# Optimization experiments

Measured on AMD Instinct MI355X. Metric: run time of the kernel, lower is better.

## Reference

```python
import jax, jax.numpy as jnp
import numpy as np

N, IN_DIM, H_DIM, POS_DIM, K, M, E, OUT_DIM = 50000, 256, 96, 32, 64, 128, 800000, 40
HID = H_DIM + POS_DIM  # 128

def _lin(key, fan_out, fan_in):
    k1, k2 = jax.random.split(key)
    bnd = 1.0 / np.sqrt(fan_in)
    W = jax.random.uniform(k1, (fan_out, fan_in), minval=-bnd, maxval=bnd, dtype=jnp.float32)
    b = jax.random.uniform(k2, (fan_out,), minval=-bnd, maxval=bnd, dtype=jnp.float32)
    return W, b

def setup_inputs() -> dict:
    key = jax.random.key(0)
    ks = jax.random.split(key, 12)
    x = jax.random.normal(ks[0], (N, IN_DIM), dtype=jnp.float32)
    eigenvectors = jax.random.normal(ks[1], (N, M), dtype=jnp.float32)
    eigenvalues = jax.random.uniform(ks[2], (M,), dtype=jnp.float32)
    edge_index = jax.random.randint(ks[3], (2, E), 0, N, dtype=jnp.int64)
    W_feat, b_feat = _lin(ks[4], H_DIM, IN_DIM)
    alpha = jax.random.uniform(ks[5], (K, POS_DIM), minval=-1/np.sqrt(K), maxval=1/np.sqrt(K), dtype=jnp.float32)
    Wl1, bl1 = _lin(ks[6], HID, HID)
    Wr1, _ = _lin(ks[7], HID, HID)
    Wl2, bl2 = _lin(ks[8], HID, HID)
    Wr2, _ = _lin(ks[9], HID, HID)
    W_ro, b_ro = _lin(ks[10], OUT_DIM, HID)
    return dict(x=x, eigenvectors=eigenvectors, eigenvalues=eigenvalues, edge_index=edge_index,
                W_feat=W_feat, b_feat=b_feat, alpha=alpha,
                Wl1=Wl1, bl1=bl1, Wr1=Wr1, Wl2=Wl2, bl2=bl2, Wr2=Wr2,
                W_ro=W_ro, b_ro=b_ro)

def _sage_conv(x, src, dst, Wl, bl, Wr):
    # PyG SAGEConv (mean aggr): out = lin_l(mean_{j->i} x_j) + lin_r(x_i)
    n = x.shape[0]
    agg = jax.ops.segment_sum(x[src], dst, num_segments=n)           # [N, HID]
    cnt = jax.ops.segment_sum(jnp.ones_like(dst, dtype=x.dtype), dst, num_segments=n)
    mean = agg / jnp.maximum(cnt, 1.0)[:, None]
    return mean @ Wl.T + bl + x @ Wr.T

def reference(x, eigenvectors, eigenvalues, edge_index,
              W_feat, b_feat, alpha, Wl1, bl1, Wr1, Wl2, bl2, Wr2, W_ro, b_ro):
    # normalize eigenvectors per column to [-1, 1]
    ev_min = jnp.min(eigenvectors, axis=0, keepdims=True)
    ev_max = jnp.max(eigenvectors, axis=0, keepdims=True)
    ev = (eigenvectors - ev_min) / (ev_max - ev_min) * 2.0 - 1.0
    # normalize eigenvalues to [-1, 1], Chebyshev basis via arccos/cos
    lmin, lmax = jnp.min(eigenvalues), jnp.max(eigenvalues)
    lam = (eigenvalues - lmin) / (lmax - lmin) * 2.0 - 1.0
    theta = jnp.arccos(lam)[:, None] * jnp.arange(K, dtype=lam.dtype)[None, :]  # [M, K]
    pe = jnp.cos(theta) @ alpha                                                  # [M, pos_dim]
    pos = ev @ pe                                                                # [N, pos_dim]
    h = jnp.concatenate([x @ W_feat.T + b_feat, pos], axis=-1)                   # [N, HID]
    src, dst = edge_index[0], edge_index[1]
    h = jax.nn.relu(_sage_conv(h, src, dst, Wl1, bl1, Wr1))
    h = jax.nn.relu(_sage_conv(h, src, dst, Wl2, bl2, Wr2))
    out = jax.nn.log_softmax(h @ W_ro.T + b_ro, axis=-1)
    return out, pe
```

## Files before the change

kernel.cpp:

```cpp
#include <hip/hip_runtime.h>
#include <math.h>

#define N        50000
#define IN_DIM   256
#define H_DIM    96
#define POS_DIM  32
#define KCH      64
#define M        128
#define NE       800000
#define OUT_DIM  40
#define HID      128
#define NSCAN    196
#define NTILES   ((N + 63) / 64)
#define NBK      391
#define BKCAP    2560
#define NSCATB   512
#define SREG     1563

typedef __attribute__((ext_vector_type(8))) short short8v;
typedef __attribute__((ext_vector_type(4))) float float4v;

__device__ __forceinline__ unsigned short f2bf(float f){
  unsigned u = __float_as_uint(f);
  u += 0x7fffu + ((u >> 16) & 1u);
  return (unsigned short)(u >> 16);
}
__device__ __forceinline__ float bf_lo(unsigned u){ return __uint_as_float(u << 16); }
__device__ __forceinline__ float bf_hi(unsigned u){ return __uint_as_float(u & 0xffff0000u); }

__device__ __forceinline__ unsigned enc_key(float f){
  unsigned u = __float_as_uint(f);
  return (u & 0x80000000u) ? ~u : (u | 0x80000000u);
}
__device__ __forceinline__ float dec_key(unsigned k){
  unsigned u = (k & 0x80000000u) ? (k ^ 0x80000000u) : ~k;
  return __uint_as_float(u);
}

__global__ void k_init(unsigned* __restrict__ encmn, unsigned* __restrict__ encmx,
                       short* __restrict__ WT_pos, float* __restrict__ bias_pos,
                       int* __restrict__ bkt_cnt){
  int i = blockIdx.x*blockDim.x + threadIdx.x;
  if (i < M){ encmn[i] = 0xFFFFFFFFu; encmx[i] = 0u; bias_pos[i] = 0.f; }
  if (i < M*M) WT_pos[i] = 0;
  if (i < NBK) bkt_cnt[i] = 0;
}

__global__ __launch_bounds__(256) void k_colminmax(const float* __restrict__ ev,
    unsigned* __restrict__ encmn, unsigned* __restrict__ encmx){
  __shared__ float4 smn[256], smx[256];
  int tid = threadIdx.x;
  int cg  = tid & 31;
  int rs  = blockIdx.x*8 + (tid >> 5);
  int stride = gridDim.x*8;
  float4 mn = make_float4( 3.4e38f,  3.4e38f,  3.4e38f,  3.4e38f);
  float4 mx = make_float4(-3.4e38f, -3.4e38f, -3.4e38f, -3.4e38f);
  #pragma unroll 4
  for (int r = rs; r < N; r += stride){
    float4 v = *(const float4*)&ev[(size_t)r*M + cg*4];
    mn.x = fminf(mn.x, v.x); mn.y = fminf(mn.y, v.y);
    mn.z = fminf(mn.z, v.z); mn.w = fminf(mn.w, v.w);
    mx.x = fmaxf(mx.x, v.x); mx.y = fmaxf(mx.y, v.y);
    mx.z = fmaxf(mx.z, v.z); mx.w = fmaxf(mx.w, v.w);
  }
  smn[tid] = mn; smx[tid] = mx;
  __syncthreads();
  for (int s = 128; s >= 32; s >>= 1){
    if (tid < s){
      float4 a = smn[tid], b = smn[tid + s];
      smn[tid] = make_float4(fminf(a.x,b.x), fminf(a.y,b.y), fminf(a.z,b.z), fminf(a.w,b.w));
      float4 c = smx[tid], d = smx[tid + s];
      smx[tid] = make_float4(fmaxf(c.x,d.x), fmaxf(c.y,d.y), fmaxf(c.z,d.z), fmaxf(c.w,d.w));
    }
    __syncthreads();
  }
  if (tid < 32){
    float4 a = smn[tid], b = smx[tid];
    atomicMin(&encmn[tid*4+0], enc_key(a.x));
    atomicMin(&encmn[tid*4+1], enc_key(a.y));
    atomicMin(&encmn[tid*4+2], enc_key(a.z));
    atomicMin(&encmn[tid*4+3], enc_key(a.w));
    atomicMax(&encmx[tid*4+0], enc_key(b.x));
    atomicMax(&encmx[tid*4+1], enc_key(b.y));
    atomicMax(&encmx[tid*4+2], enc_key(b.z));
    atomicMax(&encmx[tid*4+3], enc_key(b.w));
  }
}

__global__ __launch_bounds__(256) void k_pe(
    const float* __restrict__ eigval, const float* __restrict__ alpha,
    const unsigned* __restrict__ encmn, const unsigned* __restrict__ encmx,
    short* __restrict__ WT_pos, float* __restrict__ pe_raw,
    float* __restrict__ pe_out){
  __shared__ float rmn[128], rmx[128];
  int tid = threadIdx.x;
  if (tid < 128){ float v = eigval[tid]; rmn[tid] = v; rmx[tid] = v; }
  __syncthreads();
  for (int s = 64; s; s >>= 1){
    if (tid < s){ rmn[tid] = fminf(rmn[tid], rmn[tid+s]); rmx[tid] = fmaxf(rmx[tid], rmx[tid+s]); }
    __syncthreads();
  }
  float lmin = rmn[0], lmax = rmx[0];
  int g = blockIdx.x*256 + tid;
  int m = g >> 5, p = g & 31;
  float v = eigval[m];
  float lam = (v - lmin)/(lmax - lmin)*2.0f - 1.0f;
  lam = fminf(1.0f, fmaxf(-1.0f, lam));
  float t0 = 1.0f, t1 = lam;
  float acc = alpha[p] + lam*alpha[POS_DIM + p];
  float two_lam = lam + lam;
  #pragma unroll
  for (int k = 2; k < KCH; ++k){
    float t2 = fmaf(two_lam, t1, -t0);
    acc = fmaf(t2, alpha[k*POS_DIM + p], acc);
    t0 = t1; t1 = t2;
  }
  pe_out[g] = acc;
  pe_raw[g] = acc;
  float cmn = dec_key(encmn[m]);
  float cmx = dec_key(encmx[m]);
  float A = 2.0f/(cmx - cmn);
  WT_pos[p*M + m] = (short)f2bf(A*acc);
}

__global__ __launch_bounds__(256) void k_bias(
    const unsigned* __restrict__ encmn, const unsigned* __restrict__ encmx,
    const float* __restrict__ pe_raw, float* __restrict__ bias_pos){
  __shared__ float s[256];
  int tid = threadIdx.x;
  int p = tid >> 3, c = tid & 7;
  float sum = 0.f;
  for (int m = c*16; m < c*16 + 16; ++m){
    float cmn = dec_key(encmn[m]);
    float cmx = dec_key(encmx[m]);
    float A = 2.0f/(cmx - cmn);
    float B = -cmn*A - 1.0f;
    sum += B*pe_raw[m*POS_DIM + p];
  }
  s[tid] = sum;
  __syncthreads();
  if (c == 0){
    float t = 0.f;
    #pragma unroll
    for (int j = 0; j < 8; ++j) t += s[p*8 + j];
    bias_pos[p] = t;
  }
}

__global__ void k_prep_w(const float* __restrict__ Wf, const float* __restrict__ bfeat,
                         const float* __restrict__ Wl1, const float* __restrict__ Wr1,
                         const float* __restrict__ Wl2, const float* __restrict__ Wr2,
                         const float* __restrict__ Wro, const float* __restrict__ bro,
                         short* __restrict__ WTf, float* __restrict__ biasf,
                         short* __restrict__ Wc1, short* __restrict__ Wc2,
                         short* __restrict__ WTro, float* __restrict__ biasro){
  int i = blockIdx.x*256 + threadIdx.x;
  if (i < 128*256){
    int c = i >> 8, k = i & 255;
    WTf[i] = (c < H_DIM) ? (short)f2bf(Wf[c*IN_DIM + k]) : (short)0;
    Wc1[i] = (short)f2bf((k < HID) ? Wl1[c*HID + k] : Wr1[c*HID + k - HID]);
    Wc2[i] = (short)f2bf((k < HID) ? Wl2[c*HID + k] : Wr2[c*HID + k - HID]);
  }
  if (i < 48*128){
    int c = i >> 7, k = i & 127;
    WTro[i] = (c < OUT_DIM) ? (short)f2bf(Wro[c*HID + k]) : (short)0;
  }
  if (i < 128) biasf[i] = (i < H_DIM) ? bfeat[i] : 0.f;
  if (i >= 128 && i < 176) biasro[i - 128] = (i - 128 < OUT_DIM) ? bro[i - 128] : 0.f;
}

__global__ __launch_bounds__(256) void k_gemm_in(
    const float* __restrict__ x, const float* __restrict__ ev,
    const short* __restrict__ WTf, const float* __restrict__ biasf,
    const short* __restrict__ WT_pos, const float* __restrict__ bias_pos,
    unsigned short* __restrict__ outp)
{
  __shared__ short a_lds[64*384];
  int tid = threadIdx.x;
  int wid = tid >> 6, lane = tid & 63;
  int lrow = lane & 15, lk = (lane >> 4)*8;
  bool isPos = (wid == 3);

  short8v bfragF[8][2];
  short8v bfragP[4][2];
  float b0, b1;
  if (!isPos){
    int colBase = wid*32;
    #pragma unroll
    for (int s = 0; s < 8; ++s)
      #pragma unroll
      for (int ct = 0; ct < 2; ++ct){
        int col = colBase + ct*16 + lrow;
        bfragF[s][ct] = *(const short8v*)&WTf[col*256 + s*32 + lk];
      }
    b0 = biasf[colBase + lrow]; b1 = biasf[colBase + 16 + lrow];
  } else {
    #pragma unroll
    for (int s = 0; s < 4; ++s)
      #pragma unroll
      for (int ct = 0; ct < 2; ++ct){
        int col = ct*16 + lrow;
        bfragP[s][ct] = *(const short8v*)&WT_pos[col*128 + s*32 + lk];
      }
    b0 = bias_pos[lrow]; b1 = bias_pos[16 + lrow];
  }

  for (int tile = blockIdx.x; tile < NTILES; tile += gridDim.x){
    int n0 = tile*64;
    __syncthreads();
    for (int c = tid; c < 64*48; c += 256){
      int row = c / 48, k8 = c % 48;
      int gn = min(n0 + row, N-1);
      const float* src = (k8 < 32) ? &x[(size_t)gn*IN_DIM + k8*8]
                                   : &ev[(size_t)gn*M + (k8-32)*8];
      float4v f0 = *(const float4v*)src;
      float4v f1 = *(const float4v*)(src + 4);
      short8v vv;
      vv[0] = (short)f2bf(f0[0]); vv[1] = (short)f2bf(f0[1]);
      vv[2] = (short)f2bf(f0[2]); vv[3] = (short)f2bf(f0[3]);
      vv[4] = (short)f2bf(f1[0]); vv[5] = (short)f2bf(f1[1]);
      vv[6] = (short)f2bf(f1[2]); vv[7] = (short)f2bf(f1[3]);
      unsigned off = (unsigned)(row*768 + k8*16) ^ (unsigned)((row & 7) << 4);
      *(short8v*)((char*)a_lds + off) = vv;
    }
    __syncthreads();
    float4v acc[4][2];
    #pragma unroll
    for (int nt = 0; nt < 4; ++nt){
      acc[nt][0] = (float4v){0.f,0.f,0.f,0.f};
      acc[nt][1] = (float4v){0.f,0.f,0.f,0.f};
    }
    if (!isPos){
      #pragma unroll
      for (int s = 0; s < 8; ++s)
        #pragma unroll
        for (int nt = 0; nt < 4; ++nt){
          int row = nt*16 + lrow;
          unsigned off = (unsigned)(row*768 + (s*32 + lk)*2) ^ (unsigned)((row & 7) << 4);
          short8v a = *(const short8v*)((const char*)a_lds + off);
          acc[nt][0] = __builtin_amdgcn_mfma_f32_16x16x32_bf16(a, bfragF[s][0], acc[nt][0], 0, 0, 0);
          acc[nt][1] = __builtin_amdgcn_mfma_f32_16x16x32_bf16(a, bfragF[s][1], acc[nt][1], 0, 0, 0);
        }
    } else {
      #pragma unroll
      for (int s = 0; s < 4; ++s)
        #pragma unroll
        for (int nt = 0; nt < 4; ++nt){
          int row = nt*16 + lrow;
          unsigned off = (unsigned)(row*768 + 512 + (s*32 + lk)*2) ^ (unsigned)((row & 7) << 4);
          short8v a = *(const short8v*)((const char*)a_lds + off);
          acc[nt][0] = __builtin_amdgcn_mfma_f32_16x16x32_bf16(a, bfragP[s][0], acc[nt][0], 0, 0, 0);
          acc[nt][1] = __builtin_amdgcn_mfma_f32_16x16x32_bf16(a, bfragP[s][1], acc[nt][1], 0, 0, 0);
        }
    }
    int colBase = isPos ? 96 : wid*32;
    int rbase = (lane >> 4)*4;
    #pragma unroll
    for (int nt = 0; nt < 4; ++nt)
      #pragma unroll
      for (int ct = 0; ct < 2; ++ct){
        int col = colBase + ct*16 + lrow;
        float bb = ct ? b1 : b0;
        #pragma unroll
        for (int r = 0; r < 4; ++r){
          int node = n0 + nt*16 + rbase + r;
          if (node < N) outp[(size_t)node*HID + col] = f2bf(acc[nt][ct][r] + bb);
        }
      }
  }
}

__global__ __launch_bounds__(256) void k_conv(
    const short* __restrict__ A0, const short* __restrict__ A1,
    const short* __restrict__ WT, const float* __restrict__ bias,
    unsigned short* __restrict__ outp)
{
  __shared__ short a_lds[64*256];
  int tid = threadIdx.x;
  int wid = tid >> 6, lane = tid & 63;
  int colBase = wid*32;
  int lrow = lane & 15, lk = (lane >> 4)*8;

  short8v bfrag[8][2];
  #pragma unroll
  for (int s = 0; s < 8; ++s)
    #pragma unroll
    for (int ct = 0; ct < 2; ++ct){
      int col = colBase + ct*16 + lrow;
      bfrag[s][ct] = *(const short8v*)&WT[col*256 + s*32 + lk];
    }
  float b0 = bias[colBase + lrow], b1 = bias[colBase + 16 + lrow];

  for (int tile = blockIdx.x; tile < NTILES; tile += gridDim.x){
    int n0 = tile*64;
    __syncthreads();
    #pragma unroll
    for (int c = tid; c < 64*32; c += 256){
      int row = c >> 5, k8 = c & 31;
      int gn = min(n0 + row, N-1);
      const short* src = (k8 < 16) ? (A0 + (size_t)gn*HID + k8*8)
                                   : (A1 + (size_t)gn*HID + (k8-16)*8);
      short8v vv = *(const short8v*)src;
      unsigned off = (unsigned)(row*512 + k8*16) ^ (unsigned)((row & 7) << 4);
      *(short8v*)((char*)a_lds + off) = vv;
    }
    __syncthreads();
    float4v acc[4][2];
    #pragma unroll
    for (int nt = 0; nt < 4; ++nt){
      acc[nt][0] = (float4v){0.f,0.f,0.f,0.f};
      acc[nt][1] = (float4v){0.f,0.f,0.f,0.f};
    }
    #pragma unroll
    for (int s = 0; s < 8; ++s)
      #pragma unroll
      for (int nt = 0; nt < 4; ++nt){
        int row = nt*16 + lrow;
        unsigned off = (unsigned)(row*512 + (s*32 + lk)*2) ^ (unsigned)((row & 7) << 4);
        short8v a = *(const short8v*)((const char*)a_lds + off);
        acc[nt][0] = __builtin_amdgcn_mfma_f32_16x16x32_bf16(a, bfrag[s][0], acc[nt][0], 0, 0, 0);
        acc[nt][1] = __builtin_amdgcn_mfma_f32_16x16x32_bf16(a, bfrag[s][1], acc[nt][1], 0, 0, 0);
      }
    int rbase = (lane >> 4)*4;
    #pragma unroll
    for (int nt = 0; nt < 4; ++nt)
      #pragma unroll
      for (int ct = 0; ct < 2; ++ct){
        int col = colBase + ct*16 + lrow;
        float bb = ct ? b1 : b0;
        #pragma unroll
        for (int r = 0; r < 4; ++r){
          int node = n0 + nt*16 + rbase + r;
          if (node < N)
            outp[(size_t)node*HID + col] = f2bf(fmaxf(acc[nt][ct][r] + bb, 0.f));
        }
      }
  }
}

__global__ __launch_bounds__(256) void k_conv_ro(
    const short* __restrict__ A0, const short* __restrict__ A1,
    const short* __restrict__ WT, const float* __restrict__ bias,
    const short* __restrict__ WTro, const float* __restrict__ biasro,
    float* __restrict__ out)
{
  __shared__ short a_lds[64*256];
  __shared__ short o_lds[64*128];
  int tid = threadIdx.x;
  int wid = tid >> 6, lane = tid & 63;
  int colBase = wid*32;
  int lrow = lane & 15, lk = (lane >> 4)*8;

  short8v bfrag[8][2];
  #pragma unroll
  for (int s = 0; s < 8; ++s)
    #pragma unroll
    for (int ct = 0; ct < 2; ++ct){
      int col = colBase + ct*16 + lrow;
      bfrag[s][ct] = *(const short8v*)&WT[col*256 + s*32 + lk];
    }
  float b0 = bias[colBase + lrow], b1 = bias[colBase + 16 + lrow];

  short8v bfragR[4][3];
  #pragma unroll
  for (int s = 0; s < 4; ++s)
    #pragma unroll
    for (int t = 0; t < 3; ++t){
      int col = t*16 + lrow;
      bfragR[s][t] = *(const short8v*)&WTro[col*HID + s*32 + lk];
    }
  float biasR[3] = { biasro[lrow], biasro[16 + lrow], biasro[32 + lrow] };
  bool val2 = lrow < 8;

  for (int tile = blockIdx.x; tile < NTILES; tile += gridDim.x){
    int n0 = tile*64;
    __syncthreads();
    #pragma unroll
    for (int c = tid; c < 64*32; c += 256){
      int row = c >> 5, k8 = c & 31;
      int gn = min(n0 + row, N-1);
      const short* src = (k8 < 16) ? (A0 + (size_t)gn*HID + k8*8)
                                   : (A1 + (size_t)gn*HID + (k8-16)*8);
      short8v vv = *(const short8v*)src;
      unsigned off = (unsigned)(row*512 + k8*16) ^ (unsigned)((row & 7) << 4);
      *(short8v*)((char*)a_lds + off) = vv;
    }
    __syncthreads();
    float4v acc[4][2];
    #pragma unroll
    for (int nt = 0; nt < 4; ++nt){
      acc[nt][0] = (float4v){0.f,0.f,0.f,0.f};
      acc[nt][1] = (float4v){0.f,0.f,0.f,0.f};
    }
    #pragma unroll
    for (int s = 0; s < 8; ++s)
      #pragma unroll
      for (int nt = 0; nt < 4; ++nt){
        int row = nt*16 + lrow;
        unsigned off = (unsigned)(row*512 + (s*32 + lk)*2) ^ (unsigned)((row & 7) << 4);
        short8v a = *(const short8v*)((const char*)a_lds + off);
        acc[nt][0] = __builtin_amdgcn_mfma_f32_16x16x32_bf16(a, bfrag[s][0], acc[nt][0], 0, 0, 0);
        acc[nt][1] = __builtin_amdgcn_mfma_f32_16x16x32_bf16(a, bfrag[s][1], acc[nt][1], 0, 0, 0);
      }
    int rbase = (lane >> 4)*4;
    #pragma unroll
    for (int nt = 0; nt < 4; ++nt)
      #pragma unroll
      for (int ct = 0; ct < 2; ++ct){
        int col = colBase + ct*16 + lrow;
        float bb = ct ? b1 : b0;
        #pragma unroll
        for (int r = 0; r < 4; ++r){
          int row = nt*16 + rbase + r;
          float v = fmaxf(acc[nt][ct][r] + bb, 0.f);
          unsigned off = (unsigned)(row*256 + col*2) ^ (unsigned)((row & 7) << 4);
          *(short*)((char*)o_lds + off) = (short)f2bf(v);
        }
      }
    __syncthreads();
    float4v acc3[3];
    acc3[0] = (float4v){0.f,0.f,0.f,0.f};
    acc3[1] = (float4v){0.f,0.f,0.f,0.f};
    acc3[2] = (float4v){0.f,0.f,0.f,0.f};
    #pragma unroll
    for (int s = 0; s < 4; ++s){
      int row = wid*16 + lrow;
      unsigned off = (unsigned)(row*256 + (s*32 + lk)*2) ^ (unsigned)((row & 7) << 4);
      short8v a = *(const short8v*)((const char*)o_lds + off);
      acc3[0] = __builtin_amdgcn_mfma_f32_16x16x32_bf16(a, bfragR[s][0], acc3[0], 0, 0, 0);
      acc3[1] = __builtin_amdgcn_mfma_f32_16x16x32_bf16(a, bfragR[s][1], acc3[1], 0, 0, 0);
      acc3[2] = __builtin_amdgcn_mfma_f32_16x16x32_bf16(a, bfragR[s][2], acc3[2], 0, 0, 0);
    }
    #pragma unroll
    for (int r = 0; r < 4; ++r){
      float v0 = acc3[0][r] + biasR[0];
      float v1 = acc3[1][r] + biasR[1];
      float v2 = acc3[2][r] + biasR[2];
      float mx = fmaxf(v0, v1);
      mx = fmaxf(mx, val2 ? v2 : -3.4e38f);
      #pragma unroll
      for (int off = 1; off < 16; off <<= 1) mx = fmaxf(mx, __shfl_xor(mx, off, 64));
      float e = expf(v0 - mx) + expf(v1 - mx) + (val2 ? expf(v2 - mx) : 0.f);
      #pragma unroll
      for (int off = 1; off < 16; off <<= 1) e += __shfl_xor(e, off, 64);
      float lz = mx + logf(e);
      int node = n0 + wid*16 + (lane >> 4)*4 + r;
      if (node < N){
        out[(size_t)node*OUT_DIM + lrow]      = v0 - lz;
        out[(size_t)node*OUT_DIM + 16 + lrow] = v1 - lz;
        if (val2) out[(size_t)node*OUT_DIM + 32 + lrow] = v2 - lz;
      }
    }
  }
}

__global__ __launch_bounds__(256) void k_hist(const int* __restrict__ dst,
                                              int* __restrict__ bkt_cnt){
  __shared__ int h[NBK];
  int tid = threadIdx.x;
  for (int i = tid; i < NBK; i += 256) h[i] = 0;
  __syncthreads();
  for (int e = blockIdx.x*256 + tid; e < NE; e += gridDim.x*256)
    atomicAdd(&h[dst[e] >> 7], 1);
  __syncthreads();
  for (int i = tid; i < NBK; i += 256){
    int c = h[i];
    if (c) atomicAdd(&bkt_cnt[i], c);
  }
}

__global__ __launch_bounds__(512) void k_bktscan(const int* __restrict__ bkt_cnt,
    int* __restrict__ bkt_start, int* __restrict__ bkt_cursor){
  __shared__ int s[512];
  int t = threadIdx.x;
  int v = (t < NBK) ? bkt_cnt[t] : 0;
  s[t] = v;
  __syncthreads();
  for (int st = 1; st < 512; st <<= 1){
    int a = (t >= st) ? s[t-st] : 0;
    __syncthreads();
    s[t] += a;
    __syncthreads();
  }
  int excl = s[t] - v;
  if (t < NBK){ bkt_start[t] = excl; bkt_cursor[t] = excl; }
  if (t == 0) bkt_start[NBK] = NE;
}

__global__ __launch_bounds__(256) void k_bscatter(const int* __restrict__ src,
    const int* __restrict__ dst, int* __restrict__ bkt_cursor,
    unsigned* __restrict__ estage){
  __shared__ int lcnt[NBK];
  __shared__ int lbase[NBK];
  int tid = threadIdx.x;
  int e0 = blockIdx.x*SREG;
  int e1 = min(e0 + SREG, NE);
  for (int i = tid; i < NBK; i += 256) lcnt[i] = 0;
  __syncthreads();
  for (int e = e0 + tid; e < e1; e += 256)
    atomicAdd(&lcnt[dst[e] >> 7], 1);
  __syncthreads();
  for (int i = tid; i < NBK; i += 256){
    int c = lcnt[i];
    lbase[i] = c ? atomicAdd(&bkt_cursor[i], c) : 0;
    lcnt[i] = 0;
  }
  __syncthreads();
  for (int e = e0 + tid; e < e1; e += 256){
    int d = dst[e];
    int b = d >> 7;
    int slot = lbase[b] + atomicAdd(&lcnt[b], 1);
    estage[slot] = (unsigned)src[e] | ((unsigned)(d & 127) << 16);
  }
}

__global__ __launch_bounds__(256) void k_bcsr(const int* __restrict__ bkt_start,
    const unsigned* __restrict__ estage, unsigned short* __restrict__ csr,
    int* __restrict__ row_ptr){
  __shared__ unsigned eb[BKCAP];
  __shared__ int ncnt[128], sc[128], noff[128];
  int tid = threadIdx.x;
  int b = blockIdx.x;
  int s = bkt_start[b], e = bkt_start[b+1];
  int cnt = min(e - s, BKCAP);
  for (int i = tid; i < cnt; i += 256) eb[i] = estage[s + i];
  if (tid < 128) ncnt[tid] = 0;
  __syncthreads();
  for (int i = tid; i < cnt; i += 256)
    atomicAdd(&ncnt[(eb[i] >> 16) & 127], 1);
  __syncthreads();
  if (tid < 128) sc[tid] = ncnt[tid];
  __syncthreads();
  for (int st = 1; st < 128; st <<= 1){
    int a = (tid < 128 && tid >= st) ? sc[tid-st] : 0;
    __syncthreads();
    if (tid < 128) sc[tid] += a;
    __syncthreads();
  }
  if (tid < 128){
    int excl = sc[tid] - ncnt[tid];
    noff[tid] = excl;
    int node = b*128 + tid;
    if (node <= N) row_ptr[node] = s + excl;
    ncnt[tid] = 0;
  }
  __syncthreads();
  for (int i = tid; i < cnt; i += 256){
    unsigned v = eb[i];
    int ld = (v >> 16) & 127;
    int slot = noff[ld] + atomicAdd(&ncnt[ld], 1);
    csr[s + slot] = (unsigned short)(v & 0xffffu);
  }
}

__global__ __launch_bounds__(256) void k_agg_b(const unsigned* __restrict__ h,
    const int* __restrict__ row_ptr, const unsigned short* __restrict__ csr,
    unsigned* __restrict__ outm){
  int gid = blockIdx.x*blockDim.x + threadIdx.x;
  int i = gid >> 6;
  int lane = gid & 63;
  if (i >= N) return;
  int grp = lane >> 4;
  int lc  = lane & 15;
  int b = row_ptr[i], e = row_ptr[i+1];
  float a0[8] = {0.f,0.f,0.f,0.f,0.f,0.f,0.f,0.f};
  float a1[8] = {0.f,0.f,0.f,0.f,0.f,0.f,0.f,0.f};
  int j = b + grp;
  for (; j + 4 < e; j += 8){
    int s0 = csr[j];
    int s1 = csr[j+4];
    uint4 v0 = *(const uint4*)&h[(size_t)s0*64 + lc*4];
    uint4 v1 = *(const uint4*)&h[(size_t)s1*64 + lc*4];
    a0[0] += bf_lo(v0.x); a0[1] += bf_hi(v0.x);
    a0[2] += bf_lo(v0.y); a0[3] += bf_hi(v0.y);
    a0[4] += bf_lo(v0.z); a0[5] += bf_hi(v0.z);
    a0[6] += bf_lo(v0.w); a0[7] += bf_hi(v0.w);
    a1[0] += bf_lo(v1.x); a1[1] += bf_hi(v1.x);
    a1[2] += bf_lo(v1.y); a1[3] += bf_hi(v1.y);
    a1[4] += bf_lo(v1.z); a1[5] += bf_hi(v1.z);
    a1[6] += bf_lo(v1.w); a1[7] += bf_hi(v1.w);
  }
  if (j < e){
    int s0 = csr[j];
    uint4 v0 = *(const uint4*)&h[(size_t)s0*64 + lc*4];
    a0[0] += bf_lo(v0.x); a0[1] += bf_hi(v0.x);
    a0[2] += bf_lo(v0.y); a0[3] += bf_hi(v0.y);
    a0[4] += bf_lo(v0.z); a0[5] += bf_hi(v0.z);
    a0[6] += bf_lo(v0.w); a0[7] += bf_hi(v0.w);
  }
  #pragma unroll
  for (int k = 0; k < 8; ++k){
    float t = a0[k] + a1[k];
    t += __shfl_xor(t, 16, 64);
    t += __shfl_xor(t, 32, 64);
    a0[k] = t;
  }
  if (grp == 0){
    float inv = 1.0f / fmaxf((float)(e - b), 1.0f);
    uint4 o;
    o.x = (unsigned)f2bf(a0[0]*inv) | ((unsigned)f2bf(a0[1]*inv) << 16);
    o.y = (unsigned)f2bf(a0[2]*inv) | ((unsigned)f2bf(a0[3]*inv) << 16);
    o.z = (unsigned)f2bf(a0[4]*inv) | ((unsigned)f2bf(a0[5]*inv) << 16);
    o.w = (unsigned)f2bf(a0[6]*inv) | ((unsigned)f2bf(a0[7]*inv) << 16);
    *(uint4*)&outm[(size_t)i*64 + lc*4] = o;
  }
}

extern "C" void kernel_launch(void* const* d_in, const int* in_sizes, int n_in,
                              void* d_out, int out_size, void* d_ws, size_t ws_size,
                              hipStream_t stream){
  const float* x     = (const float*)d_in[0];
  const float* ev    = (const float*)d_in[1];
  const float* eigv  = (const float*)d_in[2];
  const int*   ei    = (const int*)d_in[3];
  const float* Wf    = (const float*)d_in[4];
  const float* bf    = (const float*)d_in[5];
  const float* alpha = (const float*)d_in[6];
  const float* Wl1   = (const float*)d_in[7];
  const float* bl1   = (const float*)d_in[8];
  const float* Wr1   = (const float*)d_in[9];
  const float* Wl2   = (const float*)d_in[10];
  const float* bl2   = (const float*)d_in[11];
  const float* Wr2   = (const float*)d_in[12];
  const float* Wro   = (const float*)d_in[13];
  const float* bro   = (const float*)d_in[14];
  float* out = (float*)d_out;

  short* h0b    = (short*)d_ws;
  short* h1b    = h0b + (size_t)N*HID;
  short* meanb  = h1b + (size_t)N*HID;
  short* WTf    = meanb + (size_t)N*HID;
  short* Wc1    = WTf + 128*256;
  short* Wc2    = Wc1 + 128*256;
  short* WT_pos = Wc2 + 128*256;
  short* WTro   = WT_pos + 128*128;
  float* biasf    = (float*)(WTro + 48*128);
  float* bias_pos = biasf + 128;
  float* biasro   = bias_pos + 128;
  unsigned* encmn = (unsigned*)(biasro + 48);
  unsigned* encmx = encmn + M;
  int* bkt_cnt    = (int*)(encmx + M);
  int* bkt_start  = bkt_cnt + NBK;
  int* bkt_cursor = bkt_start + NBK + 1;
  int* row_ptr    = bkt_cursor + NBK;
  unsigned* estage = (unsigned*)(row_ptr + N + 1);
  unsigned short* csr = (unsigned short*)(estage + NE);
  float* pe_raw = (float*)(csr + NE);

  const int* srcA = ei;
  const int* dstA = ei + NE;

  k_init<<<NSCAN, 256, 0, stream>>>(encmn, encmx, WT_pos, bias_pos, bkt_cnt);
  k_colminmax<<<256, 256, 0, stream>>>(ev, encmn, encmx);
  k_pe<<<16, 256, 0, stream>>>(eigv, alpha, encmn, encmx, WT_pos, pe_raw,
                               out + (size_t)N*OUT_DIM);
  k_bias<<<1, 256, 0, stream>>>(encmn, encmx, pe_raw, bias_pos);
  k_prep_w<<<128, 256, 0, stream>>>(Wf, bf, Wl1, Wr1, Wl2, Wr2, Wro, bro,
                                    WTf, biasf, Wc1, Wc2, WTro, biasro);
  k_hist<<<512, 256, 0, stream>>>(dstA, bkt_cnt);
  k_bktscan<<<1, 512, 0, stream>>>(bkt_cnt, bkt_start, bkt_cursor);
  k_bscatter<<<NSCATB, 256, 0, stream>>>(srcA, dstA, bkt_cursor, estage);
  k_bcsr<<<NBK, 256, 0, stream>>>(bkt_start, estage, csr, row_ptr);
  k_gemm_in<<<NTILES, 256, 0, stream>>>(x, ev, WTf, biasf, WT_pos, bias_pos,
                                        (unsigned short*)h0b);
  k_agg_b<<<(N*64)/256, 256, 0, stream>>>((const unsigned*)h0b, row_ptr, csr, (unsigned*)meanb);
  k_conv<<<NTILES, 256, 0, stream>>>(meanb, h0b, Wc1, bl1, (unsigned short*)h1b);
  k_agg_b<<<(N*64)/256, 256, 0, stream>>>((const unsigned*)h1b, row_ptr, csr, (unsigned*)meanb);
  k_conv_ro<<<NTILES, 256, 0, stream>>>(meanb, h1b, Wc2, bl2, WTro, biasro, out);
}
```

Baseline: 225.4 us.

## Merge independent preprocessing kernels into block-partitioned fused launches; unroll aggregation deeper

Independent preprocessing stages are combined into shared launches, with blocks split by blockIdx: column min/max with the edge histogram, PE/weight prep with the bucket scan, scatter with the bias reduction, and CSR build with the input GEMM. This cuts the launch count from 11 to 5 before aggregation, which reduces launch gaps and lets small kernels run alongside larger ones. The aggregation kernel now keeps four independent neighbour loads in flight instead of two to raise memory-level parallelism. In exchange, the fused blocks are heterogeneous and bring larger LDS and register footprints, and the GEMM now runs with a grid-stride offset.

```diff
diff --git a/kernel.cpp b/kernel.cpp
--- a/kernel.cpp
+++ b/kernel.cpp
@@ -38,145 +38,240 @@
 }
 
 __global__ void k_init(unsigned* __restrict__ encmn, unsigned* __restrict__ encmx,
-                       short* __restrict__ WT_pos, float* __restrict__ bias_pos,
-                       int* __restrict__ bkt_cnt){
+                       short* __restrict__ WT_pos, int* __restrict__ bkt_cnt){
   int i = blockIdx.x*blockDim.x + threadIdx.x;
-  if (i < M){ encmn[i] = 0xFFFFFFFFu; encmx[i] = 0u; bias_pos[i] = 0.f; }
+  if (i < M){ encmn[i] = 0xFFFFFFFFu; encmx[i] = 0u; }
   if (i < M*M) WT_pos[i] = 0;
   if (i < NBK) bkt_cnt[i] = 0;
 }
 
-__global__ __launch_bounds__(256) void k_colminmax(const float* __restrict__ ev,
-    unsigned* __restrict__ encmn, unsigned* __restrict__ encmx){
-  __shared__ float4 smn[256], smx[256];
+__global__ __launch_bounds__(256) void k_f1(const float* __restrict__ ev,
+    unsigned* __restrict__ encmn, unsigned* __restrict__ encmx,
+    const int* __restrict__ dst, int* __restrict__ bkt_cnt){
   int tid = threadIdx.x;
-  int cg  = tid & 31;
-  int rs  = blockIdx.x*8 + (tid >> 5);
-  int stride = gridDim.x*8;
-  float4 mn = make_float4( 3.4e38f,  3.4e38f,  3.4e38f,  3.4e38f);
-  float4 mx = make_float4(-3.4e38f, -3.4e38f, -3.4e38f, -3.4e38f);
-  #pragma unroll 4
-  for (int r = rs; r < N; r += stride){
-    float4 v = *(const float4*)&ev[(size_t)r*M + cg*4];
-    mn.x = fminf(mn.x, v.x); mn.y = fminf(mn.y, v.y);
-    mn.z = fminf(mn.z, v.z); mn.w = fminf(mn.w, v.w);
-    mx.x = fmaxf(mx.x, v.x); mx.y = fmaxf(mx.y, v.y);
-    mx.z = fmaxf(mx.z, v.z); mx.w = fmaxf(mx.w, v.w);
-  }
-  smn[tid] = mn; smx[tid] = mx;
-  __syncthreads();
-  for (int s = 128; s >= 32; s >>= 1){
-    if (tid < s){
-      float4 a = smn[tid], b = smn[tid + s];
-      smn[tid] = make_float4(fminf(a.x,b.x), fminf(a.y,b.y), fminf(a.z,b.z), fminf(a.w,b.w));
-      float4 c = smx[tid], d = smx[tid + s];
-      smx[tid] = make_float4(fmaxf(c.x,d.x), fmaxf(c.y,d.y), fmaxf(c.z,d.z), fmaxf(c.w,d.w));
-    }
-    __syncthreads();
-  }
-  if (tid < 32){
-    float4 a = smn[tid], b = smx[tid];
-    atomicMin(&encmn[tid*4+0], enc_key(a.x));
-    atomicMin(&encmn[tid*4+1], enc_key(a.y));
-    atomicMin(&encmn[tid*4+2], enc_key(a.z));
-    atomicMin(&encmn[tid*4+3], enc_key(a.w));
-    atomicMax(&encmx[tid*4+0], enc_key(b.x));
-    atomicMax(&encmx[tid*4+1], enc_key(b.y));
-    atomicMax(&encmx[tid*4+2], enc_key(b.z));
-    atomicMax(&encmx[tid*4+3], enc_key(b.w));
-  }
-}
-
-__global__ __launch_bounds__(256) void k_pe(
+  if (blockIdx.x < 256){
+    __shared__ float4 smn[256], smx[256];
+    int cg  = tid & 31;
+    int rs  = blockIdx.x*8 + (tid >> 5);
+    float4 mn = make_float4( 3.4e38f,  3.4e38f,  3.4e38f,  3.4e38f);
+    float4 mx = make_float4(-3.4e38f, -3.4e38f, -3.4e38f, -3.4e38f);
+    #pragma unroll 4
+    for (int r = rs; r < N; r += 2048){
+      float4 v = *(const float4*)&ev[(size_t)r*M + cg*4];
+      mn.x = fminf(mn.x, v.x); mn.y = fminf(mn.y, v.y);
+      mn.z = fminf(mn.z, v.z); mn.w = fminf(mn.w, v.w);
+      mx.x = fmaxf(mx.x, v.x); mx.y = fmaxf(mx.y, v.y);
+      mx.z = fmaxf(mx.z, v.z); mx.w = fmaxf(mx.w, v.w);
+    }
+    smn[tid] = mn; smx[tid] = mx;
+    __syncthreads();
+    for (int s = 128; s >= 32; s >>= 1){
+      if (tid < s){
+        float4 a = smn[tid], b = smn[tid + s];
+        smn[tid] = make_float4(fminf(a.x,b.x), fminf(a.y,b.y), fminf(a.z,b.z), fminf(a.w,b.w));
+        float4 c = smx[tid], d = smx[tid + s];
+        smx[tid] = make_float4(fmaxf(c.x,d.x), fmaxf(c.y,d.y), fmaxf(c.z,d.z), fmaxf(c.w,d.w));
+      }
+      __syncthreads();
+    }
+    if (tid < 32){
+      float4 a = smn[tid], b = smx[tid];
+      atomicMin(&encmn[tid*4+0], enc_key(a.x));
+      atomicMin(&encmn[tid*4+1], enc_key(a.y));
+      atomicMin(&encmn[tid*4+2], enc_key(a.z));
+      atomicMin(&encmn[tid*4+3], enc_key(a.w));
+      atomicMax(&encmx[tid*4+0], enc_key(b.x));
+      atomicMax(&encmx[tid*4+1], enc_key(b.y));
+      atomicMax(&encmx[tid*4+2], enc_key(b.z));
+      atomicMax(&encmx[tid*4+3], enc_key(b.w));
+    }
+  } else {
+    __shared__ int hh[NBK];
+    int bid = blockIdx.x - 256;
+    for (int i = tid; i < NBK; i += 256) hh[i] = 0;
+    __syncthreads();
+    for (int e = bid*256 + tid; e < NE; e += 512*256)
+      atomicAdd(&hh[dst[e] >> 7], 1);
+    __syncthreads();
+    for (int i = tid; i < NBK; i += 256){
+      int c = hh[i];
+      if (c) atomicAdd(&bkt_cnt[i], c);
+    }
+  }
+}
+
+__global__ __launch_bounds__(512) void k_f2(
     const float* __restrict__ eigval, const float* __restrict__ alpha,
     const unsigned* __restrict__ encmn, const unsigned* __restrict__ encmx,
-    short* __restrict__ WT_pos, float* __restrict__ pe_raw,
-    float* __restrict__ pe_out){
-  __shared__ float rmn[128], rmx[128];
+    const float* __restrict__ Wf, const float* __restrict__ bfeat,
+    const float* __restrict__ Wl1, const float* __restrict__ Wr1,
+    const float* __restrict__ Wl2, const float* __restrict__ Wr2,
+    const float* __restrict__ Wro, const float* __restrict__ bro,
+    short* __restrict__ WT_pos, float* __restrict__ pe_raw, float* __restrict__ pe_out,
+    short* __restrict__ WTf, float* __restrict__ biasf,
+    short* __restrict__ Wc1, short* __restrict__ Wc2,
+    short* __restrict__ WTro, float* __restrict__ biasro,
+    const int* __restrict__ bkt_cnt, int* __restrict__ bkt_start,
+    int* __restrict__ bkt_cursor){
   int tid = threadIdx.x;
-  if (tid < 128){ float v = eigval[tid]; rmn[tid] = v; rmx[tid] = v; }
-  __syncthreads();
-  for (int s = 64; s; s >>= 1){
-    if (tid < s){ rmn[tid] = fminf(rmn[tid], rmn[tid+s]); rmx[tid] = fmaxf(rmx[tid], rmx[tid+s]); }
-    __syncthreads();
-  }
-  float lmin = rmn[0], lmax = rmx[0];
-  int g = blockIdx.x*256 + tid;
-  int m = g >> 5, p = g & 31;
-  float v = eigval[m];
-  float lam = (v - lmin)/(lmax - lmin)*2.0f - 1.0f;
-  lam = fminf(1.0f, fmaxf(-1.0f, lam));
-  float t0 = 1.0f, t1 = lam;
-  float acc = alpha[p] + lam*alpha[POS_DIM + p];
-  float two_lam = lam + lam;
-  #pragma unroll
-  for (int k = 2; k < KCH; ++k){
-    float t2 = fmaf(two_lam, t1, -t0);
-    acc = fmaf(t2, alpha[k*POS_DIM + p], acc);
-    t0 = t1; t1 = t2;
-  }
-  pe_out[g] = acc;
-  pe_raw[g] = acc;
-  float cmn = dec_key(encmn[m]);
-  float cmx = dec_key(encmx[m]);
-  float A = 2.0f/(cmx - cmn);
-  WT_pos[p*M + m] = (short)f2bf(A*acc);
-}
-
-__global__ __launch_bounds__(256) void k_bias(
-    const unsigned* __restrict__ encmn, const unsigned* __restrict__ encmx,
-    const float* __restrict__ pe_raw, float* __restrict__ bias_pos){
-  __shared__ float s[256];
-  int tid = threadIdx.x;
-  int p = tid >> 3, c = tid & 7;
-  float sum = 0.f;
-  for (int m = c*16; m < c*16 + 16; ++m){
+  if (blockIdx.x < 8){
+    __shared__ float rmn[128], rmx[128];
+    if (tid < 128){ float v = eigval[tid]; rmn[tid] = v; rmx[tid] = v; }
+    __syncthreads();
+    for (int s = 64; s; s >>= 1){
+      if (tid < s){ rmn[tid] = fminf(rmn[tid], rmn[tid+s]); rmx[tid] = fmaxf(rmx[tid], rmx[tid+s]); }
+      __syncthreads();
+    }
+    float lmin = rmn[0], lmax = rmx[0];
+    int g = blockIdx.x*512 + tid;
+    int m = g >> 5, p = g & 31;
+    float v = eigval[m];
+    float lam = (v - lmin)/(lmax - lmin)*2.0f - 1.0f;
+    lam = fminf(1.0f, fmaxf(-1.0f, lam));
+    float t0 = 1.0f, t1 = lam;
+    float acc = alpha[p] + lam*alpha[POS_DIM + p];
+    float two_lam = lam + lam;
+    #pragma unroll
+    for (int k = 2; k < KCH; ++k){
+      float t2 = fmaf(two_lam, t1, -t0);
+      acc = fmaf(t2, alpha[k*POS_DIM + p], acc);
+      t0 = t1; t1 = t2;
+    }
+    pe_out[g] = acc;
+    pe_raw[g] = acc;
     float cmn = dec_key(encmn[m]);
     float cmx = dec_key(encmx[m]);
     float A = 2.0f/(cmx - cmn);
-    float B = -cmn*A - 1.0f;
-    sum += B*pe_raw[m*POS_DIM + p];
-  }
-  s[tid] = sum;
-  __syncthreads();
-  if (c == 0){
-    float t = 0.f;
-    #pragma unroll
-    for (int j = 0; j < 8; ++j) t += s[p*8 + j];
-    bias_pos[p] = t;
-  }
-}
-
-__global__ void k_prep_w(const float* __restrict__ Wf, const float* __restrict__ bfeat,
-                         const float* __restrict__ Wl1, const float* __restrict__ Wr1,
-                         const float* __restrict__ Wl2, const float* __restrict__ Wr2,
-                         const float* __restrict__ Wro, const float* __restrict__ bro,
-                         short* __restrict__ WTf, float* __restrict__ biasf,
-                         short* __restrict__ Wc1, short* __restrict__ Wc2,
-                         short* __restrict__ WTro, float* __restrict__ biasro){
-  int i = blockIdx.x*256 + threadIdx.x;
-  if (i < 128*256){
-    int c = i >> 8, k = i & 255;
-    WTf[i] = (c < H_DIM) ? (short)f2bf(Wf[c*IN_DIM + k]) : (short)0;
-    Wc1[i] = (short)f2bf((k < HID) ? Wl1[c*HID + k] : Wr1[c*HID + k - HID]);
-    Wc2[i] = (short)f2bf((k < HID) ? Wl2[c*HID + k] : Wr2[c*HID + k - HID]);
-  }
-  if (i < 48*128){
-    int c = i >> 7, k = i & 127;
-    WTro[i] = (c < OUT_DIM) ? (short)f2bf(Wro[c*HID + k]) : (short)0;
-  }
-  if (i < 128) biasf[i] = (i < H_DIM) ? bfeat[i] : 0.f;
-  if (i >= 128 && i < 176) biasro[i - 128] = (i - 128 < OUT_DIM) ? bro[i - 128] : 0.f;
-}
-
-__global__ __launch_bounds__(256) void k_gemm_in(
+    WT_pos[p*M + m] = (short)f2bf(A*acc);
+    for (int i = g; i < 128*256; i += 4096){
+      int c = i >> 8, k = i & 255;
+      WTf[i] = (c < H_DIM) ? (short)f2bf(Wf[c*IN_DIM + k]) : (short)0;
+      Wc1[i] = (short)f2bf((k < HID) ? Wl1[c*HID + k] : Wr1[c*HID + k - HID]);
+      Wc2[i] = (short)f2bf((k < HID) ? Wl2[c*HID + k] : Wr2[c*HID + k - HID]);
+    }
+    for (int i = g; i < 48*128; i += 4096){
+      int c = i >> 7, k = i & 127;
+      WTro[i] = (c < OUT_DIM) ? (short)f2bf(Wro[c*HID + k]) : (short)0;
+    }
+    if (g < 128) biasf[g] = (g < H_DIM) ? bfeat[g] : 0.f;
+    if (g >= 128 && g < 176) biasro[g - 128] = (g - 128 < OUT_DIM) ? bro[g - 128] : 0.f;
+  } else {
+    __shared__ int s[512];
+    int t = tid;
+    int v = (t < NBK) ? bkt_cnt[t] : 0;
+    s[t] = v;
+    __syncthreads();
+    for (int st = 1; st < 512; st <<= 1){
+      int a = (t >= st) ? s[t-st] : 0;
+      __syncthreads();
+      s[t] += a;
+      __syncthreads();
+    }
+    int excl = s[t] - v;
+    if (t < NBK){ bkt_start[t] = excl; bkt_cursor[t] = excl; }
+    if (t == 0) bkt_start[NBK] = NE;
+  }
+}
+
+__global__ __launch_bounds__(256) void k_f3(const int* __restrict__ src,
+    const int* __restrict__ dst, int* __restrict__ bkt_cursor,
+    unsigned* __restrict__ estage,
+    const unsigned* __restrict__ encmn, const unsigned* __restrict__ encmx,
+    const float* __restrict__ pe_raw, float* __restrict__ bias_pos){
+  int tid = threadIdx.x;
+  if (blockIdx.x < NSCATB){
+    __shared__ int lcnt[NBK];
+    __shared__ int lbase[NBK];
+    int e0 = blockIdx.x*SREG;
+    int e1 = min(e0 + SREG, NE);
+    for (int i = tid; i < NBK; i += 256) lcnt[i] = 0;
+    __syncthreads();
+    for (int e = e0 + tid; e < e1; e += 256)
+      atomicAdd(&lcnt[dst[e] >> 7], 1);
+    __syncthreads();
+    for (int i = tid; i < NBK; i += 256){
+      int c = lcnt[i];
+      lbase[i] = c ? atomicAdd(&bkt_cursor[i], c) : 0;
+      lcnt[i] = 0;
+    }
+    __syncthreads();
+    for (int e = e0 + tid; e < e1; e += 256){
+      int d = dst[e];
+      int b = d >> 7;
+      int slot = lbase[b] + atomicAdd(&lcnt[b], 1);
+      estage[slot] = (unsigned)src[e] | ((unsigned)(d & 127) << 16);
+    }
+  } else {
+    __shared__ float s[256];
+    int p = tid >> 3, c = tid & 7;
+    float sum = 0.f;
+    for (int m = c*16; m < c*16 + 16; ++m){
+      float cmn = dec_key(encmn[m]);
+      float cmx = dec_key(encmx[m]);
+      float A = 2.0f/(cmx - cmn);
+      float B = -cmn*A - 1.0f;
+      sum += B*pe_raw[m*POS_DIM + p];
+    }
+    s[tid] = sum;
+    __syncthreads();
+    if (c == 0){
+      float t = 0.f;
+      #pragma unroll
+      for (int j = 0; j < 8; ++j) t += s[p*8 + j];
+      bias_pos[p] = t;
+    }
+  }
+}
+
+__global__ __launch_bounds__(256) void k_f4(
+    const int* __restrict__ bkt_start, const unsigned* __restrict__ estage,
+    unsigned short* __restrict__ csr, int* __restrict__ row_ptr,
     const float* __restrict__ x, const float* __restrict__ ev,
     const short* __restrict__ WTf, const float* __restrict__ biasf,
     const short* __restrict__ WT_pos, const float* __restrict__ bias_pos,
     unsigned short* __restrict__ outp)
 {
-  __shared__ short a_lds[64*384];
+  __shared__ __align__(16) char smem[64*384*2];
   int tid = threadIdx.x;
+  if (blockIdx.x < NBK){
+    unsigned* eb = (unsigned*)smem;
+    int* ncnt = (int*)(smem + BKCAP*4);
+    int* sc   = ncnt + 128;
+    int* noff = sc + 128;
+    int b = blockIdx.x;
+    int s = bkt_start[b], e = bkt_start[b+1];
+    int cnt = min(e - s, BKCAP);
+    for (int i = tid; i < cnt; i += 256) eb[i] = estage[s + i];
+    if (tid < 128) ncnt[tid] = 0;
+    __syncthreads();
+    for (int i = tid; i < cnt; i += 256)
+      atomicAdd(&ncnt[(eb[i] >> 16) & 127], 1);
+    __syncthreads();
+    if (tid < 128) sc[tid] = ncnt[tid];
+    __syncthreads();
+    for (int st = 1; st < 128; st <<= 1){
+      int a = (tid < 128 && tid >= st) ? sc[tid-st] : 0;
+      __syncthreads();
+      if (tid < 128) sc[tid] += a;
+      __syncthreads();
+    }
+    if (tid < 128){
+      int excl = sc[tid] - ncnt[tid];
+      noff[tid] = excl;
+      int node = b*128 + tid;
+      if (node <= N) row_ptr[node] = s + excl;
+      ncnt[tid] = 0;
+    }
+    __syncthreads();
+    for (int i = tid; i < cnt; i += 256){
+      unsigned v = eb[i];
+      int ld = (v >> 16) & 127;
+      int slot = noff[ld] + atomicAdd(&ncnt[ld], 1);
+      csr[s + slot] = (unsigned short)(v & 0xffffu);
+    }
+    return;
+  }
+  short* a_lds = (short*)smem;
   int wid = tid >> 6, lane = tid & 63;
   int lrow = lane & 15, lk = (lane >> 4)*8;
   bool isPos = (wid == 3);
@@ -205,7 +300,7 @@
     b0 = bias_pos[lrow]; b1 = bias_pos[16 + lrow];
   }
 
-  for (int tile = blockIdx.x; tile < NTILES; tile += gridDim.x){
+  for (int tile = blockIdx.x - NBK; tile < NTILES; tile += gridDim.x - NBK){
     int n0 = tile*64;
     __syncthreads();
     for (int c = tid; c < 64*48; c += 256){
@@ -270,6 +365,56 @@
   }
 }
 
+__global__ __launch_bounds__(256) void k_agg_b(const unsigned* __restrict__ h,
+    const int* __restrict__ row_ptr, const unsigned short* __restrict__ csr,
+    unsigned* __restrict__ outm){
+  int gid = blockIdx.x*blockDim.x + threadIdx.x;
+  int i = gid >> 6;
+  int lane = gid & 63;
+  if (i >= N) return;
+  int grp = lane >> 4;
+  int lc  = lane & 15;
+  int b = row_ptr[i], e = row_ptr[i+1];
+  float a0[8] = {0,0,0,0,0,0,0,0}, a1[8] = {0,0,0,0,0,0,0,0};
+  float a2[8] = {0,0,0,0,0,0,0,0}, a3[8] = {0,0,0,0,0,0,0,0};
+  int j = b + grp;
+  for (; j + 12 < e; j += 16){
+    uint4 v0 = *(const uint4*)&h[(size_t)csr[j]*64    + lc*4];
+    uint4 v1 = *(const uint4*)&h[(size_t)csr[j+4]*64  + lc*4];
+    uint4 v2 = *(const uint4*)&h[(size_t)csr[j+8]*64  + lc*4];
+    uint4 v3 = *(const uint4*)&h[(size_t)csr[j+12]*64 + lc*4];
+    a0[0] += bf_lo(v0.x); a0[1] += bf_hi(v0.x); a0[2] += bf_lo(v0.y); a0[3] += bf_hi(v0.y);
+    a0[4] += bf_lo(v0.z); a0[5] += bf_hi(v0.z); a0[6] += bf_lo(v0.w); a0[7] += bf_hi(v0.w);
+    a1[0] += bf_lo(v1.x); a1[1] += bf_hi(v1.x); a1[2] += bf_lo(v1.y); a1[3] += bf_hi(v1.y);
+    a1[4] += bf_lo(v1.z); a1[5] += bf_hi(v1.z); a1[6] += bf_lo(v1.w); a1[7] += bf_hi(v1.w);
+    a2[0] += bf_lo(v2.x); a2[1] += bf_hi(v2.x); a2[2] += bf_lo(v2.y); a2[3] += bf_hi(v2.y);
+    a2[4] += bf_lo(v2.z); a2[5] += bf_hi(v2.z); a2[6] += bf_lo(v2.w); a2[7] += bf_hi(v2.w);
+    a3[0] += bf_lo(v3.x); a3[1] += bf_hi(v3.x); a3[2] += bf_lo(v3.y); a3[3] += bf_hi(v3.y);
+    a3[4] += bf_lo(v3.z); a3[5] += bf_hi(v3.z); a3[6] += bf_lo(v3.w); a3[7] += bf_hi(v3.w);
+  }
+  for (; j < e; j += 4){
+    uint4 v0 = *(const uint4*)&h[(size_t)csr[j]*64 + lc*4];
+    a0[0] += bf_lo(v0.x); a0[1] += bf_hi(v0.x); a0[2] += bf_lo(v0.y); a0[3] += bf_hi(v0.y);
+    a0[4] += bf_lo(v0.z); a0[5] += bf_hi(v0.z); a0[6] += bf_lo(v0.w); a0[7] += bf_hi(v0.w);
+  }
+  #pragma unroll
+  for (int k = 0; k < 8; ++k){
+    float t = (a0[k] + a1[k]) + (a2[k] + a3[k]);
+    t += __shfl_xor(t, 16, 64);
+    t += __shfl_xor(t, 32, 64);
+    a0[k] = t;
+  }
+  if (grp == 0){
+    float inv = 1.0f / fmaxf((float)(e - b), 1.0f);
+    uint4 o;
+    o.x = (unsigned)f2bf(a0[0]*inv) | ((unsigned)f2bf(a0[1]*inv) << 16);
+    o.y = (unsigned)f2bf(a0[2]*inv) | ((unsigned)f2bf(a0[3]*inv) << 16);
+    o.z = (unsigned)f2bf(a0[4]*inv) | ((unsigned)f2bf(a0[5]*inv) << 16);
+    o.w = (unsigned)f2bf(a0[6]*inv) | ((unsigned)f2bf(a0[7]*inv) << 16);
+    *(uint4*)&outm[(size_t)i*64 + lc*4] = o;
+  }
+}
+
 __global__ __launch_bounds__(256) void k_conv(
     const short* __restrict__ A0, const short* __restrict__ A1,
     const short* __restrict__ WT, const float* __restrict__ bias,
@@ -451,158 +596,6 @@
         if (val2) out[(size_t)node*OUT_DIM + 32 + lrow] = v2 - lz;
       }
     }
-  }
-}
-
-__global__ __launch_bounds__(256) void k_hist(const int* __restrict__ dst,
-                                              int* __restrict__ bkt_cnt){
-  __shared__ int h[NBK];
-  int tid = threadIdx.x;
-  for (int i = tid; i < NBK; i += 256) h[i] = 0;
-  __syncthreads();
-  for (int e = blockIdx.x*256 + tid; e < NE; e += gridDim.x*256)
-    atomicAdd(&h[dst[e] >> 7], 1);
-  __syncthreads();
-  for (int i = tid; i < NBK; i += 256){
-    int c = h[i];
-    if (c) atomicAdd(&bkt_cnt[i], c);
-  }
-}
-
-__global__ __launch_bounds__(512) void k_bktscan(const int* __restrict__ bkt_cnt,
-    int* __restrict__ bkt_start, int* __restrict__ bkt_cursor){
-  __shared__ int s[512];
-  int t = threadIdx.x;
-  int v = (t < NBK) ? bkt_cnt[t] : 0;
-  s[t] = v;
-  __syncthreads();
-  for (int st = 1; st < 512; st <<= 1){
-    int a = (t >= st) ? s[t-st] : 0;
-    __syncthreads();
-    s[t] += a;
-    __syncthreads();
-  }
-  int excl = s[t] - v;
-  if (t < NBK){ bkt_start[t] = excl; bkt_cursor[t] = excl; }
-  if (t == 0) bkt_start[NBK] = NE;
-}
-
-__global__ __launch_bounds__(256) void k_bscatter(const int* __restrict__ src,
-    const int* __restrict__ dst, int* __restrict__ bkt_cursor,
-    unsigned* __restrict__ estage){
-  __shared__ int lcnt[NBK];
-  __shared__ int lbase[NBK];
-  int tid = threadIdx.x;
-  int e0 = blockIdx.x*SREG;
-  int e1 = min(e0 + SREG, NE);
-  for (int i = tid; i < NBK; i += 256) lcnt[i] = 0;
-  __syncthreads();
-  for (int e = e0 + tid; e < e1; e += 256)
-    atomicAdd(&lcnt[dst[e] >> 7], 1);
-  __syncthreads();
-  for (int i = tid; i < NBK; i += 256){
-    int c = lcnt[i];
-    lbase[i] = c ? atomicAdd(&bkt_cursor[i], c) : 0;
-    lcnt[i] = 0;
-  }
-  __syncthreads();
-  for (int e = e0 + tid; e < e1; e += 256){
-    int d = dst[e];
-    int b = d >> 7;
-    int slot = lbase[b] + atomicAdd(&lcnt[b], 1);
-    estage[slot] = (unsigned)src[e] | ((unsigned)(d & 127) << 16);
-  }
-}
-
-__global__ __launch_bounds__(256) void k_bcsr(const int* __restrict__ bkt_start,
-    const unsigned* __restrict__ estage, unsigned short* __restrict__ csr,
-    int* __restrict__ row_ptr){
-  __shared__ unsigned eb[BKCAP];
-  __shared__ int ncnt[128], sc[128], noff[128];
-  int tid = threadIdx.x;
-  int b = blockIdx.x;
-  int s = bkt_start[b], e = bkt_start[b+1];
-  int cnt = min(e - s, BKCAP);
-  for (int i = tid; i < cnt; i += 256) eb[i] = estage[s + i];
-  if (tid < 128) ncnt[tid] = 0;
-  __syncthreads();
-  for (int i = tid; i < cnt; i += 256)
-    atomicAdd(&ncnt[(eb[i] >> 16) & 127], 1);
-  __syncthreads();
-  if (tid < 128) sc[tid] = ncnt[tid];
-  __syncthreads();
-  for (int st = 1; st < 128; st <<= 1){
-    int a = (tid < 128 && tid >= st) ? sc[tid-st] : 0;
-    __syncthreads();
-    if (tid < 128) sc[tid] += a;
-    __syncthreads();
-  }
-  if (tid < 128){
-    int excl = sc[tid] - ncnt[tid];
-    noff[tid] = excl;
-    int node = b*128 + tid;
-    if (node <= N) row_ptr[node] = s + excl;
-    ncnt[tid] = 0;
-  }
-  __syncthreads();
-  for (int i = tid; i < cnt; i += 256){
-    unsigned v = eb[i];
-    int ld = (v >> 16) & 127;
-    int slot = noff[ld] + atomicAdd(&ncnt[ld], 1);
-    csr[s + slot] = (unsigned short)(v & 0xffffu);
-  }
-}
-
-__global__ __launch_bounds__(256) void k_agg_b(const unsigned* __restrict__ h,
-    const int* __restrict__ row_ptr, const unsigned short* __restrict__ csr,
-    unsigned* __restrict__ outm){
-  int gid = blockIdx.x*blockDim.x + threadIdx.x;
-  int i = gid >> 6;
-  int lane = gid & 63;
-  if (i >= N) return;
-  int grp = lane >> 4;
-  int lc  = lane & 15;
-  int b = row_ptr[i], e = row_ptr[i+1];
-  float a0[8] = {0.f,0.f,0.f,0.f,0.f,0.f,0.f,0.f};
-  float a1[8] = {0.f,0.f,0.f,0.f,0.f,0.f,0.f,0.f};
-  int j = b + grp;
-  for (; j + 4 < e; j += 8){
-    int s0 = csr[j];
-    int s1 = csr[j+4];
-    uint4 v0 = *(const uint4*)&h[(size_t)s0*64 + lc*4];
-    uint4 v1 = *(const uint4*)&h[(size_t)s1*64 + lc*4];
-    a0[0] += bf_lo(v0.x); a0[1] += bf_hi(v0.x);
-    a0[2] += bf_lo(v0.y); a0[3] += bf_hi(v0.y);
-    a0[4] += bf_lo(v0.z); a0[5] += bf_hi(v0.z);
-    a0[6] += bf_lo(v0.w); a0[7] += bf_hi(v0.w);
-    a1[0] += bf_lo(v1.x); a1[1] += bf_hi(v1.x);
-    a1[2] += bf_lo(v1.y); a1[3] += bf_hi(v1.y);
-    a1[4] += bf_lo(v1.z); a1[5] += bf_hi(v1.z);
-    a1[6] += bf_lo(v1.w); a1[7] += bf_hi(v1.w);
-  }
-  if (j < e){
-    int s0 = csr[j];
-    uint4 v0 = *(const uint4*)&h[(size_t)s0*64 + lc*4];
-    a0[0] += bf_lo(v0.x); a0[1] += bf_hi(v0.x);
-    a0[2] += bf_lo(v0.y); a0[3] += bf_hi(v0.y);
-    a0[4] += bf_lo(v0.z); a0[5] += bf_hi(v0.z);
-    a0[6] += bf_lo(v0.w); a0[7] += bf_hi(v0.w);
-  }
-  #pragma unroll
-  for (int k = 0; k < 8; ++k){
-    float t = a0[k] + a1[k];
-    t += __shfl_xor(t, 16, 64);
-    t += __shfl_xor(t, 32, 64);
-    a0[k] = t;
-  }
-  if (grp == 0){
-    float inv = 1.0f / fmaxf((float)(e - b), 1.0f);
-    uint4 o;
-    o.x = (unsigned)f2bf(a0[0]*inv) | ((unsigned)f2bf(a0[1]*inv) << 16);
-    o.y = (unsigned)f2bf(a0[2]*inv) | ((unsigned)f2bf(a0[3]*inv) << 16);
-    o.z = (unsigned)f2bf(a0[4]*inv) | ((unsigned)f2bf(a0[5]*inv) << 16);
-    o.w = (unsigned)f2bf(a0[6]*inv) | ((unsigned)f2bf(a0[7]*inv) << 16);
-    *(uint4*)&outm[(size_t)i*64 + lc*4] = o;
   }
 }
 
@@ -650,19 +643,18 @@
   const int* srcA = ei;
   const int* dstA = ei + NE;
 
-  k_init<<<NSCAN, 256, 0, stream>>>(encmn, encmx, WT_pos, bias_pos, bkt_cnt);
-  k_colminmax<<<256, 256, 0, stream>>>(ev, encmn, encmx);
-  k_pe<<<16, 256, 0, stream>>>(eigv, alpha, encmn, encmx, WT_pos, pe_raw,
-                               out + (size_t)N*OUT_DIM);
-  k_bias<<<1, 256, 0, stream>>>(encmn, encmx, pe_raw, bias_pos);
-  k_prep_w<<<128, 256, 0, stream>>>(Wf, bf, Wl1, Wr1, Wl2, Wr2, Wro, bro,
-                                    WTf, biasf, Wc1, Wc2, WTro, biasro);
-  k_hist<<<512, 256, 0, stream>>>(dstA, bkt_cnt);
-  k_bktscan<<<1, 512, 0, stream>>>(bkt_cnt, bkt_start, bkt_cursor);
-  k_bscatter<<<NSCATB, 256, 0, stream>>>(srcA, dstA, bkt_cursor, estage);
-  k_bcsr<<<NBK, 256, 0, stream>>>(bkt_start, estage, csr, row_ptr);
-  k_gemm_in<<<NTILES, 256, 0, stream>>>(x, ev, WTf, biasf, WT_pos, bias_pos,
-                                        (unsigned short*)h0b);
+  k_init<<<NSCAN, 256, 0, stream>>>(encmn, encmx, WT_pos, bkt_cnt);
+  k_f1<<<768, 256, 0, stream>>>(ev, encmn, encmx, dstA, bkt_cnt);
+  k_f2<<<9, 512, 0, stream>>>(eigv, alpha, encmn, encmx,
+                              Wf, bf, Wl1, Wr1, Wl2, Wr2, Wro, bro,
+                              WT_pos, pe_raw, out + (size_t)N*OUT_DIM,
+                              WTf, biasf, Wc1, Wc2, WTro, biasro,
+                              bkt_cnt, bkt_start, bkt_cursor);
+  k_f3<<<NSCATB + 1, 256, 0, stream>>>(srcA, dstA, bkt_cursor, estage,
+                                       encmn, encmx, pe_raw, bias_pos);
+  k_f4<<<NBK + NTILES, 256, 0, stream>>>(bkt_start, estage, csr, row_ptr,
+                                         x, ev, WTf, biasf, WT_pos, bias_pos,
+                                         (unsigned short*)h0b);
   k_agg_b<<<(N*64)/256, 256, 0, stream>>>((const unsigned*)h0b, row_ptr, csr, (unsigned*)meanb);
   k_conv<<<NTILES, 256, 0, stream>>>(meanb, h0b, Wc1, bl1, (unsigned short*)h1b);
   k_agg_b<<<(N*64)/256, 256, 0, stream>>>((const unsigned*)h1b, row_ptr, csr, (unsigned*)meanb);
```

After: 210.9 us. -6.4%, faster.
